# Kernel tuning notes

Hardware: AMD Instinct MI355X
Metric: run time of the kernel (lower is better)

## Reference

```python
import jax, jax.numpy as jnp
import numpy as np

N = 100000
E = 3200000
D = 128
H = 128
Q = 1000000
EPS = 1e-6


def _lin_params(key, fan_in, fan_out):
    k1, k2 = jax.random.split(key)
    bound = 1.0 / np.sqrt(fan_in)
    W = jax.random.uniform(k1, (fan_out, fan_in), jnp.float32, -bound, bound)
    b = jax.random.uniform(k2, (fan_out,), jnp.float32, -bound, bound)
    return W, b


def setup_inputs() -> dict:
    key = jax.random.key(0)
    ks = jax.random.split(key, 10)
    x = jax.random.normal(ks[0], (N, D), jnp.float32)
    edge_index = jax.random.randint(ks[1], (2, E), 0, N, jnp.int64)
    decode_index = jax.random.randint(ks[2], (2, Q), 0, N, jnp.int64)
    # SAGEConv1: lin_l (on aggregated neighbors, has bias) + lin_r (root, no bias)
    W1l, b1l = _lin_params(ks[3], D, H)
    W1r, _ = _lin_params(ks[4], D, H)
    W2l, b2l = _lin_params(ks[5], H, H)
    W2r, _ = _lin_params(ks[6], H, H)
    Wi, bi = _lin_params(ks[7], H, H)   # rnn.i2h
    Wh, bh = _lin_params(ks[8], H, H)   # rnn.h2h (applied to zero hidden -> bias only)
    Wo, bo = _lin_params(ks[9], H, H)   # rnn.h2o
    return {"x": x, "edge_index": edge_index, "decode_index": decode_index,
            "W1l": W1l, "b1l": b1l, "W1r": W1r,
            "W2l": W2l, "b2l": b2l, "W2r": W2r,
            "Wi": Wi, "bi": bi, "Wh": Wh, "bh": bh, "Wo": Wo, "bo": bo}


def _sage(x, src, dst, Wl, bl, Wr):
    # mean-aggregate source features onto targets, then lin_l(agg)+lin_r(x)
    msg = x[src]                                              # [E, d] gather
    agg = jax.ops.segment_sum(msg, dst, num_segments=N)       # [N, d] scatter-add
    cnt = jax.ops.segment_sum(jnp.ones((src.shape[0],), x.dtype), dst, num_segments=N)
    mean = agg / jnp.maximum(cnt, 1.0)[:, None]
    return mean @ Wl.T + bl + x @ Wr.T


def reference(x, edge_index, decode_index, W1l, b1l, W1r, W2l, b2l, W2r,
              Wi, bi, Wh, bh, Wo, bo):
    src, dst = edge_index[0], edge_index[1]
    h = jax.nn.relu(_sage(x, src, dst, W1l, b1l, W1r))
    # dropout is identity in eval mode
    h = _sage(h, src, dst, W2l, b2l, W2r)
    # RNN step: hidden is reset to zeros inside original forward, so h2h -> bias
    hid = jnp.tanh(h @ Wi.T + bi + bh)                        # [N, H]
    out = hid @ Wo.T + bo                                     # [N, H]
    a = out[decode_index[0]]                                  # [Q, H]
    b = out[decode_index[1]]
    na = jnp.maximum(jnp.linalg.norm(a, axis=1), EPS)
    nb = jnp.maximum(jnp.linalg.norm(b, axis=1), EPS)
    cos = jnp.sum(a * b, axis=1) / (na * nb)                  # [Q]
    return jax.nn.sigmoid(cos)
```

## Files before the change

### kernel.cpp

```cpp
#include <hip/hip_runtime.h>
#include <math.h>

#define DH 128
#define STILE 1024
#define BBLK 256
#define MAXK 512

typedef __attribute__((ext_vector_type(4))) float f32x4;
typedef __attribute__((ext_vector_type(8))) short short8;


__device__ __forceinline__ float lo2f(unsigned w) { return __uint_as_float(w << 16); }
__device__ __forceinline__ float hi2f(unsigned w) { return __uint_as_float(w & 0xFFFF0000u); }
__device__ __forceinline__ unsigned pack2bf(float a, float b) {
    unsigned ua = __float_as_uint(a), ub = __float_as_uint(b);
    unsigned ra = (ua + 0x7FFFu + ((ua >> 16) & 1u)) >> 16;
    unsigned rb = (ub + 0x7FFFu + ((ub >> 16) & 1u)) >> 16;
    return ra | (rb << 16);
}
__device__ __forceinline__ ushort bf16r(float f) {
    unsigned u = __float_as_uint(f);
    return (ushort)((u + 0x7FFFu + ((u >> 16) & 1u)) >> 16);
}

__global__ __launch_bounds__(256) void k_tobf(const float* __restrict__ in,
                                              uint4* __restrict__ outv, int n8) {
    int i = blockIdx.x * blockDim.x + threadIdx.x;
    if (i >= n8) return;
    const float4* p = reinterpret_cast<const float4*>(in);
    float4 a = p[i * 2], b = p[i * 2 + 1];
    uint4 w;
    w.x = pack2bf(a.x, a.y); w.y = pack2bf(a.z, a.w);
    w.z = pack2bf(b.x, b.y); w.w = pack2bf(b.z, b.w);
    outv[i] = w;
}


__global__ __launch_bounds__(512) void k_bhist(const int* __restrict__ ei,
                                               int* __restrict__ ghist,
                                               int E_, int K) {
    __shared__ int lh[MAXK];
    int tid = threadIdx.x, blk = blockIdx.x;
    if (tid < MAXK) lh[tid] = 0;
    __syncthreads();
    const int* dsts = ei + E_;
    int E4 = E_ >> 2;
    for (int e4 = blk * 512 + tid; e4 < E4; e4 += BBLK * 512) {
        int4 d4 = *reinterpret_cast<const int4*>(dsts + e4 * 4);
        atomicAdd(&lh[d4.x >> 8], 1);
        atomicAdd(&lh[d4.y >> 8], 1);
        atomicAdd(&lh[d4.z >> 8], 1);
        atomicAdd(&lh[d4.w >> 8], 1);
    }
    if (blk == 0 && tid < (E_ & 3)) atomicAdd(&lh[dsts[(E4 << 2) + tid] >> 8], 1);
    __syncthreads();
    if (tid < K) ghist[tid * BBLK + blk] = lh[tid];
}


__global__ __launch_bounds__(256) void k_scan1(const int* __restrict__ deg,
                                               int* __restrict__ excl,
                                               int* __restrict__ tsum, int N_) {
    __shared__ int wsum[4];
    int t = threadIdx.x;
    int idx = blockIdx.x * STILE + t * 4;
    int4 v = {0, 0, 0, 0};
    if (idx + 3 < N_) {
        v = *reinterpret_cast<const int4*>(deg + idx);
    } else {
        if (idx + 0 < N_) v.x = deg[idx + 0];
        if (idx + 1 < N_) v.y = deg[idx + 1];
        if (idx + 2 < N_) v.z = deg[idx + 2];
        if (idx + 3 < N_) v.w = deg[idx + 3];
    }
    int s0 = v.x, s1 = s0 + v.y, s2 = s1 + v.z, s3 = s2 + v.w;
    int lane = t & 63, w = t >> 6;
    int inc = s3;
    for (int off = 1; off < 64; off <<= 1) {
        int u = __shfl_up(inc, off, 64);
        if (lane >= off) inc += u;
    }
    if (lane == 63) wsum[w] = inc;
    __syncthreads();
    int woff = 0;
    for (int i = 0; i < w; ++i) woff += wsum[i];
    int exq = woff + inc - s3;
    int4 e;
    e.x = exq; e.y = exq + s0; e.z = exq + s1; e.w = exq + s2;
    if (idx + 3 < N_) {
        *reinterpret_cast<int4*>(excl + idx) = e;
    } else {
        if (idx + 0 < N_) excl[idx + 0] = e.x;
        if (idx + 1 < N_) excl[idx + 1] = e.y;
        if (idx + 2 < N_) excl[idx + 2] = e.z;
        if (idx + 3 < N_) excl[idx + 3] = e.w;
    }
    if (t == 255) tsum[blockIdx.x] = woff + inc;
}

__global__ void k_scan2(const int* __restrict__ tsum, int* __restrict__ toff,
                        int ntiles, int* __restrict__ totalOut) {
    __shared__ int sh[1024];
    int t = threadIdx.x;
    int v = (t < ntiles) ? tsum[t] : 0;
    sh[t] = v;
    __syncthreads();
    for (int off = 1; off < 1024; off <<= 1) {
        int u = (t >= off) ? sh[t - off] : 0;
        __syncthreads();
        sh[t] += u;
        __syncthreads();
    }
    if (t < ntiles) toff[t] = sh[t] - v;
    if (t == 1023) *totalOut = sh[1023];
}

__global__ __launch_bounds__(256) void k_scan3s(int* __restrict__ buf,
                                                const int* __restrict__ toff, int N_) {
    int off = toff[blockIdx.x];
    int idx = blockIdx.x * STILE + threadIdx.x * 4;
    if (idx + 3 < N_) {
        int4 e = *reinterpret_cast<int4*>(buf + idx);
        e.x += off; e.y += off; e.z += off; e.w += off;
        *reinterpret_cast<int4*>(buf + idx) = e;
    } else {
        for (int i = 0; i < 4; ++i)
            if (idx + i < N_) buf[idx + i] += off;
    }
}

__global__ __launch_bounds__(512) void k_bwrite(const int* __restrict__ ei,
                                                const int* __restrict__ goff,
                                                int2* __restrict__ ebuf,
                                                int E_, int K) {
    __shared__ int lcur[MAXK];
    int tid = threadIdx.x, blk = blockIdx.x;
    if (tid < K) lcur[tid] = goff[tid * BBLK + blk];
    __syncthreads();
    const int* dsts = ei + E_;
    int E4 = E_ >> 2;
    for (int e4 = blk * 512 + tid; e4 < E4; e4 += BBLK * 512) {
        int4 d4 = *reinterpret_cast<const int4*>(dsts + e4 * 4);
        int4 s4 = *reinterpret_cast<const int4*>(ei + e4 * 4);
        int p;
        p = atomicAdd(&lcur[d4.x >> 8], 1); ebuf[p] = make_int2(s4.x, d4.x);
        p = atomicAdd(&lcur[d4.y >> 8], 1); ebuf[p] = make_int2(s4.y, d4.y);
        p = atomicAdd(&lcur[d4.z >> 8], 1); ebuf[p] = make_int2(s4.z, d4.z);
        p = atomicAdd(&lcur[d4.w >> 8], 1); ebuf[p] = make_int2(s4.w, d4.w);
    }
    if (blk == 0 && tid < (E_ & 3)) {
        int e = (E4 << 2) + tid;
        int d = dsts[e];
        int p = atomicAdd(&lcur[d >> 8], 1);
        ebuf[p] = make_int2(ei[e], d);
    }
}

__global__ __launch_bounds__(256) void k_bscatter(const int2* __restrict__ ebuf,
                                                  const int* __restrict__ goff,
                                                  int* __restrict__ rowptr,
                                                  int* __restrict__ col,
                                                  int E_, int N_, int K) {
    __shared__ int ldeg[256], lrp[256], lcur[256], wsum[4];
    int b = blockIdx.x;
    int tid = threadIdx.x;
    int n0 = b << 8;
    int nn = min(256, N_ - n0);
    int estart = goff[b * BBLK];
    int eend = (b + 1 < K) ? goff[(b + 1) * BBLK] : E_;
    ldeg[tid] = 0;
    lcur[tid] = 0;
    __syncthreads();
    for (int e = estart + tid; e < eend; e += 256)
        atomicAdd(&ldeg[ebuf[e].y - n0], 1);
    __syncthreads();
    int v = ldeg[tid];
    int lane = tid & 63, w = tid >> 6;
    int inc = v;
    for (int off = 1; off < 64; off <<= 1) {
        int u = __shfl_up(inc, off, 64);
        if (lane >= off) inc += u;
    }
    if (lane == 63) wsum[w] = inc;
    __syncthreads();
    int woff = 0;
    for (int i = 0; i < w; ++i) woff += wsum[i];
    int rp = estart + woff + inc - v;
    lrp[tid] = rp;
    if (tid < nn) rowptr[n0 + tid] = rp;
    __syncthreads();
    for (int e = estart + tid; e < eend; e += 256) {
        int2 pr = ebuf[e];
        int dl = pr.y - n0;
        int p = lrp[dl] + atomicAdd(&lcur[dl], 1);
        col[p] = pr.x;
    }
}


__global__ __launch_bounds__(256) void k_prepw(const float* __restrict__ w0,
                                               const float* __restrict__ w1,
                                               const float* __restrict__ w2,
                                               const float* __restrict__ w3,
                                               const float* __restrict__ w4,
                                               const float* __restrict__ w5,
                                               ushort* __restrict__ wf) {
    int t = blockIdx.x * 256 + threadIdx.x;
    if (t >= 12288) return;
    int m = t >> 11;
    int rem = t & 2047;
    int kb = rem >> 9;
    int rem2 = rem & 511;
    int jb = rem2 >> 6;
    int l = rem2 & 63;
    const float* W;
    switch (m) {
        case 0: W = w0; break; case 1: W = w1; break; case 2: W = w2; break;
        case 3: W = w3; break; case 4: W = w4; break; default: W = w5; break;
    }
    int j = jb * 16 + (l & 15);
    int k0 = kb * 32 + (l >> 4) * 8;
    const float* src = W + (size_t)j * DH + k0;
    uint4 o;
    o.x = pack2bf(src[0], src[1]);
    o.y = pack2bf(src[2], src[3]);
    o.z = pack2bf(src[4], src[5]);
    o.w = pack2bf(src[6], src[7]);
    *reinterpret_cast<uint4*>(wf + (size_t)t * 8) = o;
}


__global__ __launch_bounds__(256) void k_agg_bf(const uint2* __restrict__ Fv,
                                                const int* __restrict__ rowptr,
                                                const int* __restrict__ col,
                                                uint2* __restrict__ out, int N_) {
    int g = (blockIdx.x * blockDim.x + threadIdx.x) >> 5;
    int l = threadIdx.x & 31;
    if (g >= N_) return;
    int lo = rowptr[g], hi = rowptr[g + 1];
    float4 acc0 = {0.f, 0.f, 0.f, 0.f};
    float4 acc1 = {0.f, 0.f, 0.f, 0.f};
    float4 acc2 = {0.f, 0.f, 0.f, 0.f};
    float4 acc3 = {0.f, 0.f, 0.f, 0.f};
    int j = lo;
    for (; j + 3 < hi; j += 4) {
        int s0 = col[j], s1 = col[j + 1], s2 = col[j + 2], s3 = col[j + 3];
        uint2 v0 = Fv[(size_t)s0 * 32 + l];
        uint2 v1 = Fv[(size_t)s1 * 32 + l];
        uint2 v2 = Fv[(size_t)s2 * 32 + l];
        uint2 v3 = Fv[(size_t)s3 * 32 + l];
        acc0.x += lo2f(v0.x); acc0.y += hi2f(v0.x); acc0.z += lo2f(v0.y); acc0.w += hi2f(v0.y);
        acc1.x += lo2f(v1.x); acc1.y += hi2f(v1.x); acc1.z += lo2f(v1.y); acc1.w += hi2f(v1.y);
        acc2.x += lo2f(v2.x); acc2.y += hi2f(v2.x); acc2.z += lo2f(v2.y); acc2.w += hi2f(v2.y);
        acc3.x += lo2f(v3.x); acc3.y += hi2f(v3.x); acc3.z += lo2f(v3.y); acc3.w += hi2f(v3.y);
    }
    for (; j < hi; ++j) {
        uint2 v0 = Fv[(size_t)col[j] * 32 + l];
        acc0.x += lo2f(v0.x); acc0.y += hi2f(v0.x); acc0.z += lo2f(v0.y); acc0.w += hi2f(v0.y);
    }
    float inv = 1.0f / fmaxf((float)(hi - lo), 1.0f);
    float rx = (acc0.x + acc1.x + acc2.x + acc3.x) * inv;
    float ry = (acc0.y + acc1.y + acc2.y + acc3.y) * inv;
    float rz = (acc0.z + acc1.z + acc2.z + acc3.z) * inv;
    float rw = (acc0.w + acc1.w + acc2.w + acc3.w) * inv;
    uint2 w;
    w.x = pack2bf(rx, ry);
    w.y = pack2bf(rz, rw);
    out[(size_t)g * 32 + l] = w;
}


template <int ACT>
__global__ __launch_bounds__(256) void k_mfma_dual(const ushort* __restrict__ A,
                                                   const ushort* __restrict__ B,
                                                   const ushort* __restrict__ WaF,
                                                   const ushort* __restrict__ WbF,
                                                   const float* __restrict__ bias,
                                                   ushort* __restrict__ out, int N_) {
    int wv = threadIdx.x >> 6;
    int l  = threadIdx.x & 63;
    int base = blockIdx.x * 64 + wv * 16;
    if (base >= N_) return;
    int l15 = l & 15, g = l >> 4;
    f32x4 acc[8];
#pragma unroll
    for (int jb = 0; jb < 8; ++jb) {
        float b = bias[jb * 16 + l15];
        acc[jb] = (f32x4){b, b, b, b};
    }
    const ushort* arow = A + (size_t)(base + l15) * DH + g * 8;
    const ushort* brow = B + (size_t)(base + l15) * DH + g * 8;
#pragma unroll
    for (int kb = 0; kb < 4; ++kb) {
        short8 aA = *reinterpret_cast<const short8*>(arow + kb * 32);
        short8 aB = *reinterpret_cast<const short8*>(brow + kb * 32);
        const ushort* wa = WaF + kb * 4096 + l * 8;
        const ushort* wb = WbF + kb * 4096 + l * 8;
#pragma unroll
        for (int jb = 0; jb < 8; ++jb) {
            short8 fa = *reinterpret_cast<const short8*>(wa + jb * 512);
            short8 fb = *reinterpret_cast<const short8*>(wb + jb * 512);
            acc[jb] = __builtin_amdgcn_mfma_f32_16x16x32_bf16(aA, fa, acc[jb], 0, 0, 0);
            acc[jb] = __builtin_amdgcn_mfma_f32_16x16x32_bf16(aB, fb, acc[jb], 0, 0, 0);
        }
    }
    ushort* orow = out + (size_t)(base + g * 4) * DH + l15;
#pragma unroll
    for (int jb = 0; jb < 8; ++jb) {
#pragma unroll
        for (int r = 0; r < 4; ++r) {
            float v = acc[jb][r];
            if (ACT) v = fmaxf(v, 0.f);
            orow[(size_t)r * DH + jb * 16] = bf16r(v);
        }
    }
}


__global__ __launch_bounds__(256) void k_rnn_mfma(const ushort* __restrict__ H2,
                                                  const ushort* __restrict__ WiF,
                                                  const float* __restrict__ bi,
                                                  const float* __restrict__ bh,
                                                  const ushort* __restrict__ WoF,
                                                  const float* __restrict__ bo,
                                                  ushort* __restrict__ out, int N_) {
    __shared__ ushort lds[4][16][136];
    int wv = threadIdx.x >> 6;
    int l  = threadIdx.x & 63;
    int base = blockIdx.x * 64 + wv * 16;
    if (base >= N_) return;
    int l15 = l & 15, g = l >> 4;
    f32x4 acc[8];
#pragma unroll
    for (int jb = 0; jb < 8; ++jb) {
        float b = bi[jb * 16 + l15] + bh[jb * 16 + l15];
        acc[jb] = (f32x4){b, b, b, b};
    }
    const ushort* arow = H2 + (size_t)(base + l15) * DH + g * 8;
#pragma unroll
    for (int kb = 0; kb < 4; ++kb) {
        short8 a = *reinterpret_cast<const short8*>(arow + kb * 32);
        const ushort* wi = WiF + kb * 4096 + l * 8;
#pragma unroll
        for (int jb = 0; jb < 8; ++jb) {
            short8 f = *reinterpret_cast<const short8*>(wi + jb * 512);
            acc[jb] = __builtin_amdgcn_mfma_f32_16x16x32_bf16(a, f, acc[jb], 0, 0, 0);
        }
    }
#pragma unroll
    for (int jb = 0; jb < 8; ++jb)
#pragma unroll
        for (int r = 0; r < 4; ++r)
            lds[wv][g * 4 + r][jb * 16 + l15] = bf16r(tanhf(acc[jb][r]));
#pragma unroll
    for (int jb = 0; jb < 8; ++jb) {
        float b = bo[jb * 16 + l15];
        acc[jb] = (f32x4){b, b, b, b};
    }
#pragma unroll
    for (int kb = 0; kb < 4; ++kb) {
        short8 a = *reinterpret_cast<const short8*>(&lds[wv][l15][kb * 32 + g * 8]);
        const ushort* wo = WoF + kb * 4096 + l * 8;
#pragma unroll
        for (int jb = 0; jb < 8; ++jb) {
            short8 f = *reinterpret_cast<const short8*>(wo + jb * 512);
            acc[jb] = __builtin_amdgcn_mfma_f32_16x16x32_bf16(a, f, acc[jb], 0, 0, 0);
        }
    }
#pragma unroll
    for (int r = 0; r < 4; ++r) {
        float ss = 0.f;
#pragma unroll
        for (int jb = 0; jb < 8; ++jb) ss += acc[jb][r] * acc[jb][r];
        ss += __shfl_xor(ss, 1);
        ss += __shfl_xor(ss, 2);
        ss += __shfl_xor(ss, 4);
        ss += __shfl_xor(ss, 8);
        float inv = 1.0f / fmaxf(sqrtf(ss), 1e-6f);
        ushort* orow = out + (size_t)(base + g * 4 + r) * DH + l15;
#pragma unroll
        for (int jb = 0; jb < 8; ++jb)
            orow[jb * 16] = bf16r(acc[jb][r] * inv);
    }
}


__global__ __launch_bounds__(256) void k_decode(const uint2* __restrict__ Fn,
                                                const int* __restrict__ di,
                                                float* __restrict__ res, int Q_) {
    int q = (blockIdx.x * blockDim.x + threadIdx.x) >> 5;
    int l = threadIdx.x & 31;
    if (q >= Q_) return;
    int ia = di[q];
    int ib = di[Q_ + q];
    uint2 a = Fn[(size_t)ia * 32 + l];
    uint2 b = Fn[(size_t)ib * 32 + l];
    float s = lo2f(a.x) * lo2f(b.x) + hi2f(a.x) * hi2f(b.x)
            + lo2f(a.y) * lo2f(b.y) + hi2f(a.y) * hi2f(b.y);
#pragma unroll
    for (int off = 16; off; off >>= 1) s += __shfl_xor(s, off, 32);
    if (l == 0) res[q] = 1.0f / (1.0f + expf(-s));
}


extern "C" void kernel_launch(void* const* d_in, const int* in_sizes, int n_in,
                              void* d_out, int out_size, void* d_ws, size_t ws_size,
                              hipStream_t stream) {
    const float* x   = (const float*)d_in[0];
    const int*   ei  = (const int*)d_in[1];
    const int*   di  = (const int*)d_in[2];
    const float* W1l = (const float*)d_in[3];
    const float* b1l = (const float*)d_in[4];
    const float* W1r = (const float*)d_in[5];
    const float* W2l = (const float*)d_in[6];
    const float* b2l = (const float*)d_in[7];
    const float* W2r = (const float*)d_in[8];
    const float* Wi  = (const float*)d_in[9];
    const float* bi  = (const float*)d_in[10];
    const float* bh  = (const float*)d_in[12];
    const float* Wo  = (const float*)d_in[13];
    const float* bo  = (const float*)d_in[14];
    float* outq = (float*)d_out;

    int N_ = in_sizes[0] / DH;
    int E_ = in_sizes[1] / 2;
    int Q_ = in_sizes[2] / 2;
    int K  = (N_ + 255) >> 8;
    int GH = K * BBLK;
    int gtiles = (GH + STILE - 1) / STILE;

    char* base = (char*)d_ws;
    size_t o = 0;
    auto alloc = [&](size_t bytes) -> void* {
        o = (o + 511) & ~(size_t)511;
        void* p = base + o;
        o += bytes;
        return p;
    };
    int*    rowptr = (int*)alloc((size_t)(N_ + 1) * 4);
    int*    col    = (int*)alloc((size_t)E_ * 4);
    int*    ghist  = (int*)alloc((size_t)GH * 4);
    int*    goff   = (int*)alloc((size_t)GH * 4);
    int2*   ebuf   = (int2*)alloc((size_t)E_ * 8);
    int*    tsum   = (int*)alloc((size_t)1024 * 4);
    int*    toff   = (int*)alloc((size_t)1024 * 4);
    ushort* wf     = (ushort*)alloc((size_t)6 * 16384 * 2);
    void*   xbf    = alloc((size_t)N_ * DH * 2);
    void*   hbf    = alloc((size_t)N_ * DH * 2);
    void*   aggbf  = alloc((size_t)N_ * DH * 2);
    void*   h2bf   = alloc((size_t)N_ * DH * 2);
    void*   outbf  = alloc((size_t)N_ * DH * 2);

    k_tobf<<<(N_ * DH / 8 + 255) / 256, 256, 0, stream>>>(x, (uint4*)xbf, N_ * DH / 8);
    k_bhist<<<BBLK, 512, 0, stream>>>(ei, ghist, E_, K);
    k_scan1<<<gtiles, 256, 0, stream>>>(ghist, goff, tsum, GH);
    k_scan2<<<1, 1024, 0, stream>>>(tsum, toff, gtiles, rowptr + N_);
    k_scan3s<<<gtiles, 256, 0, stream>>>(goff, toff, GH);
    k_bwrite<<<BBLK, 512, 0, stream>>>(ei, goff, ebuf, E_, K);
    k_bscatter<<<K, 256, 0, stream>>>(ebuf, goff, rowptr, col, E_, N_, K);
    k_prepw<<<48, 256, 0, stream>>>(W1l, W1r, W2l, W2r, Wi, Wo, wf);

    int gw = (N_ + 63) / 64;
    k_agg_bf<<<(N_ + 7) / 8, 256, 0, stream>>>((const uint2*)xbf, rowptr, col, (uint2*)aggbf, N_);
    k_mfma_dual<1><<<gw, 256, 0, stream>>>((const ushort*)aggbf, (const ushort*)xbf,
                                           wf + 0 * 16384, wf + 1 * 16384, b1l,
                                           (ushort*)hbf, N_);
    k_agg_bf<<<(N_ + 7) / 8, 256, 0, stream>>>((const uint2*)hbf, rowptr, col, (uint2*)aggbf, N_);
    k_mfma_dual<0><<<gw, 256, 0, stream>>>((const ushort*)aggbf, (const ushort*)hbf,
                                           wf + 2 * 16384, wf + 3 * 16384, b2l,
                                           (ushort*)h2bf, N_);
    k_rnn_mfma<<<gw, 256, 0, stream>>>((const ushort*)h2bf, wf + 4 * 16384, bi, bh,
                                       wf + 5 * 16384, bo, (ushort*)outbf, N_);
    k_decode<<<(Q_ + 7) / 8, 256, 0, stream>>>((const uint2*)outbf, di, outq, Q_);
}
```

Measured before the change: 609.5 us.

## Store gathered node features in FP8 for aggregation and decode gathers

Converts the node feature tables read by the neighbor-aggregation gathers and the decode gathers from bf16 to 8-bit e4m3 floats. The x conversion kernel now also emits an fp8 copy, a new pass quantizes the layer-1 output to fp8, and the RNN kernel writes its normalized output in fp8. This halves the bytes moved by the random-access gathers, which dominate memory traffic. The cost is an extra quantization pass and much lower precision in the aggregated means and cosine scores, which may exceed tolerance.

New measurement: 519.0 us. 1.17x faster.

```diff
diff --git a/kernel.cpp b/kernel.cpp
--- a/kernel.cpp
+++ b/kernel.cpp
@@ -7,7 +7,14 @@
 #define MAXK 512
 
 typedef __attribute__((ext_vector_type(4))) float f32x4;
+typedef __attribute__((ext_vector_type(2))) float f32x2;
 typedef __attribute__((ext_vector_type(8))) short short8;
+
+#if __has_builtin(__builtin_amdgcn_cvt_pk_f32_fp8) && __has_builtin(__builtin_amdgcn_cvt_pk_fp8_f32)
+#define HAVE_HW_FP8 1
+#else
+#define HAVE_HW_FP8 0
+#endif
 
 
 __device__ __forceinline__ float lo2f(unsigned w) { return __uint_as_float(w << 16); }
@@ -23,8 +30,60 @@
     return (ushort)((u + 0x7FFFu + ((u >> 16) & 1u)) >> 16);
 }
 
+
+__device__ __forceinline__ float fp8tof(unsigned v) {
+    return __uint_as_float(((v & 0x80u) << 24) | ((v & 0x7Fu) << 20)) * 0x1p120f;
+}
+
+__device__ __forceinline__ unsigned f2fp8(float f) {
+    unsigned s = (__float_as_uint(f) >> 24) & 0x80u;
+    float a = fabsf(f);
+    if (a > 448.0f) a = 448.0f;
+    if (a < 0x1p-10f) return s;
+    int e = (int)((__float_as_uint(a) >> 23) & 0xFF) - 127;
+    if (e < -6) {
+        unsigned m = (unsigned)rintf(a * 512.0f);
+        return s | m;
+    }
+    unsigned ua = __float_as_uint(a);
+    unsigned em = (unsigned)(((e + 7) << 3) | ((ua >> 20) & 7u));
+    unsigned rest = ua & 0xFFFFFu;
+    em += (rest > 0x80000u) || (rest == 0x80000u && (em & 1u));
+    if (em > 0x7Eu) em = 0x7Eu;
+    return s | em;
+}
+
+__device__ __forceinline__ unsigned pack4q(float x0, float x1, float x2, float x3) {
+#if HAVE_HW_FP8
+    int v = __builtin_amdgcn_cvt_pk_fp8_f32(x0, x1, 0, false);
+    v = __builtin_amdgcn_cvt_pk_fp8_f32(x2, x3, v, true);
+    return (unsigned)v;
+#else
+    return f2fp8(x0) | (f2fp8(x1) << 8) | (f2fp8(x2) << 16) | (f2fp8(x3) << 24);
+#endif
+}
+
+__device__ __forceinline__ void unpack4q(unsigned u, float& f0, float& f1, float& f2, float& f3) {
+#if HAVE_HW_FP8
+    f32x2 lo = __builtin_amdgcn_cvt_pk_f32_fp8((int)u, false);
+    f32x2 hi = __builtin_amdgcn_cvt_pk_f32_fp8((int)u, true);
+    f0 = lo[0]; f1 = lo[1]; f2 = hi[0]; f3 = hi[1];
+#else
+    f0 = fp8tof(u); f1 = fp8tof(u >> 8); f2 = fp8tof(u >> 16); f3 = fp8tof(u >> 24);
+#endif
+}
+
+__device__ __forceinline__ unsigned f2q1(float v) {
+#if HAVE_HW_FP8
+    return (unsigned)__builtin_amdgcn_cvt_pk_fp8_f32(v, v, 0, false) & 0xFFu;
+#else
+    return f2fp8(v);
+#endif
+}
+
 __global__ __launch_bounds__(256) void k_tobf(const float* __restrict__ in,
-                                              uint4* __restrict__ outv, int n8) {
+                                              uint4* __restrict__ outbf,
+                                              uint2* __restrict__ outq, int n8) {
     int i = blockIdx.x * blockDim.x + threadIdx.x;
     if (i >= n8) return;
     const float4* p = reinterpret_cast<const float4*>(in);
@@ -32,7 +91,19 @@
     uint4 w;
     w.x = pack2bf(a.x, a.y); w.y = pack2bf(a.z, a.w);
     w.z = pack2bf(b.x, b.y); w.w = pack2bf(b.z, b.w);
-    outv[i] = w;
+    outbf[i] = w;
+    uint2 q;
+    q.x = pack4q(a.x, a.y, a.z, a.w);
+    q.y = pack4q(b.x, b.y, b.z, b.w);
+    outq[i] = q;
+}
+
+__global__ __launch_bounds__(256) void k_bf2q(const uint2* __restrict__ inb,
+                                              unsigned* __restrict__ outq, int n4) {
+    int i = blockIdx.x * blockDim.x + threadIdx.x;
+    if (i >= n4) return;
+    uint2 v = inb[i];
+    outq[i] = pack4q(lo2f(v.x), hi2f(v.x), lo2f(v.y), hi2f(v.y));
 }
 
 
@@ -56,7 +127,6 @@
     __syncthreads();
     if (tid < K) ghist[tid * BBLK + blk] = lh[tid];
 }
-
 
 __global__ __launch_bounds__(256) void k_scan1(const int* __restrict__ deg,
                                                int* __restrict__ excl,
@@ -230,10 +300,10 @@
 }
 
 
-__global__ __launch_bounds__(256) void k_agg_bf(const uint2* __restrict__ Fv,
-                                                const int* __restrict__ rowptr,
-                                                const int* __restrict__ col,
-                                                uint2* __restrict__ out, int N_) {
+__global__ __launch_bounds__(256) void k_agg_q(const unsigned* __restrict__ Fq,
+                                               const int* __restrict__ rowptr,
+                                               const int* __restrict__ col,
+                                               uint2* __restrict__ out, int N_) {
     int g = (blockIdx.x * blockDim.x + threadIdx.x) >> 5;
     int l = threadIdx.x & 31;
     if (g >= N_) return;
@@ -245,18 +315,25 @@
     int j = lo;
     for (; j + 3 < hi; j += 4) {
         int s0 = col[j], s1 = col[j + 1], s2 = col[j + 2], s3 = col[j + 3];
-        uint2 v0 = Fv[(size_t)s0 * 32 + l];
-        uint2 v1 = Fv[(size_t)s1 * 32 + l];
-        uint2 v2 = Fv[(size_t)s2 * 32 + l];
-        uint2 v3 = Fv[(size_t)s3 * 32 + l];
-        acc0.x += lo2f(v0.x); acc0.y += hi2f(v0.x); acc0.z += lo2f(v0.y); acc0.w += hi2f(v0.y);
-        acc1.x += lo2f(v1.x); acc1.y += hi2f(v1.x); acc1.z += lo2f(v1.y); acc1.w += hi2f(v1.y);
-        acc2.x += lo2f(v2.x); acc2.y += hi2f(v2.x); acc2.z += lo2f(v2.y); acc2.w += hi2f(v2.y);
-        acc3.x += lo2f(v3.x); acc3.y += hi2f(v3.x); acc3.z += lo2f(v3.y); acc3.w += hi2f(v3.y);
+        unsigned v0 = Fq[(size_t)s0 * 32 + l];
+        unsigned v1 = Fq[(size_t)s1 * 32 + l];
+        unsigned v2 = Fq[(size_t)s2 * 32 + l];
+        unsigned v3 = Fq[(size_t)s3 * 32 + l];
+        float f0, f1, f2, f3;
+        unpack4q(v0, f0, f1, f2, f3);
+        acc0.x += f0; acc0.y += f1; acc0.z += f2; acc0.w += f3;
+        unpack4q(v1, f0, f1, f2, f3);
+        acc1.x += f0; acc1.y += f1; acc1.z += f2; acc1.w += f3;
+        unpack4q(v2, f0, f1, f2, f3);
+        acc2.x += f0; acc2.y += f1; acc2.z += f2; acc2.w += f3;
+        unpack4q(v3, f0, f1, f2, f3);
+        acc3.x += f0; acc3.y += f1; acc3.z += f2; acc3.w += f3;
     }
     for (; j < hi; ++j) {
-        uint2 v0 = Fv[(size_t)col[j] * 32 + l];
-        acc0.x += lo2f(v0.x); acc0.y += hi2f(v0.x); acc0.z += lo2f(v0.y); acc0.w += hi2f(v0.y);
+        unsigned v0 = Fq[(size_t)col[j] * 32 + l];
+        float f0, f1, f2, f3;
+        unpack4q(v0, f0, f1, f2, f3);
+        acc0.x += f0; acc0.y += f1; acc0.z += f2; acc0.w += f3;
     }
     float inv = 1.0f / fmaxf((float)(hi - lo), 1.0f);
     float rx = (acc0.x + acc1.x + acc2.x + acc3.x) * inv;
@@ -323,7 +400,7 @@
                                                   const float* __restrict__ bh,
                                                   const ushort* __restrict__ WoF,
                                                   const float* __restrict__ bo,
-                                                  ushort* __restrict__ out, int N_) {
+                                                  unsigned char* __restrict__ outq, int N_) {
     __shared__ ushort lds[4][16][136];
     int wv = threadIdx.x >> 6;
     int l  = threadIdx.x & 63;
@@ -377,15 +454,15 @@
         ss += __shfl_xor(ss, 4);
         ss += __shfl_xor(ss, 8);
         float inv = 1.0f / fmaxf(sqrtf(ss), 1e-6f);
-        ushort* orow = out + (size_t)(base + g * 4 + r) * DH + l15;
+        unsigned char* orow = outq + (size_t)(base + g * 4 + r) * DH + l15;
 #pragma unroll
         for (int jb = 0; jb < 8; ++jb)
-            orow[jb * 16] = bf16r(acc[jb][r] * inv);
-    }
-}
-
-
-__global__ __launch_bounds__(256) void k_decode(const uint2* __restrict__ Fn,
+            orow[jb * 16] = (unsigned char)f2q1(acc[jb][r] * inv);
+    }
+}
+
+
+__global__ __launch_bounds__(256) void k_decode(const unsigned* __restrict__ Fq,
                                                 const int* __restrict__ di,
                                                 float* __restrict__ res, int Q_) {
     int q = (blockIdx.x * blockDim.x + threadIdx.x) >> 5;
@@ -393,10 +470,12 @@
     if (q >= Q_) return;
     int ia = di[q];
     int ib = di[Q_ + q];
-    uint2 a = Fn[(size_t)ia * 32 + l];
-    uint2 b = Fn[(size_t)ib * 32 + l];
-    float s = lo2f(a.x) * lo2f(b.x) + hi2f(a.x) * hi2f(b.x)
-            + lo2f(a.y) * lo2f(b.y) + hi2f(a.y) * hi2f(b.y);
+    unsigned a = Fq[(size_t)ia * 32 + l];
+    unsigned b = Fq[(size_t)ib * 32 + l];
+    float a0, a1, a2, a3, b0, b1, b2, b3;
+    unpack4q(a, a0, a1, a2, a3);
+    unpack4q(b, b0, b1, b2, b3);
+    float s = a0 * b0 + a1 * b1 + a2 * b2 + a3 * b3;
 #pragma unroll
     for (int off = 16; off; off >>= 1) s += __shfl_xor(s, off, 32);
     if (l == 0) res[q] = 1.0f / (1.0f + expf(-s));
@@ -449,9 +528,12 @@
     void*   hbf    = alloc((size_t)N_ * DH * 2);
     void*   aggbf  = alloc((size_t)N_ * DH * 2);
     void*   h2bf   = alloc((size_t)N_ * DH * 2);
-    void*   outbf  = alloc((size_t)N_ * DH * 2);
-
-    k_tobf<<<(N_ * DH / 8 + 255) / 256, 256, 0, stream>>>(x, (uint4*)xbf, N_ * DH / 8);
+    void*   xq     = alloc((size_t)N_ * DH);
+    void*   hq     = alloc((size_t)N_ * DH);
+    void*   oq     = alloc((size_t)N_ * DH);
+
+    k_tobf<<<(N_ * DH / 8 + 255) / 256, 256, 0, stream>>>(x, (uint4*)xbf, (uint2*)xq,
+                                                          N_ * DH / 8);
     k_bhist<<<BBLK, 512, 0, stream>>>(ei, ghist, E_, K);
     k_scan1<<<gtiles, 256, 0, stream>>>(ghist, goff, tsum, GH);
     k_scan2<<<1, 1024, 0, stream>>>(tsum, toff, gtiles, rowptr + N_);
@@ -461,15 +543,19 @@
     k_prepw<<<48, 256, 0, stream>>>(W1l, W1r, W2l, W2r, Wi, Wo, wf);
 
     int gw = (N_ + 63) / 64;
-    k_agg_bf<<<(N_ + 7) / 8, 256, 0, stream>>>((const uint2*)xbf, rowptr, col, (uint2*)aggbf, N_);
+    k_agg_q<<<(N_ + 7) / 8, 256, 0, stream>>>((const unsigned*)xq, rowptr, col,
+                                              (uint2*)aggbf, N_);
     k_mfma_dual<1><<<gw, 256, 0, stream>>>((const ushort*)aggbf, (const ushort*)xbf,
                                            wf + 0 * 16384, wf + 1 * 16384, b1l,
                                            (ushort*)hbf, N_);
-    k_agg_bf<<<(N_ + 7) / 8, 256, 0, stream>>>((const uint2*)hbf, rowptr, col, (uint2*)aggbf, N_);
+    k_bf2q<<<(N_ * DH / 4 + 255) / 256, 256, 0, stream>>>((const uint2*)hbf,
+                                                          (unsigned*)hq, N_ * DH / 4);
+    k_agg_q<<<(N_ + 7) / 8, 256, 0, stream>>>((const unsigned*)hq, rowptr, col,
+                                              (uint2*)aggbf, N_);
     k_mfma_dual<0><<<gw, 256, 0, stream>>>((const ushort*)aggbf, (const ushort*)hbf,
                                            wf + 2 * 16384, wf + 3 * 16384, b2l,
                                            (ushort*)h2bf, N_);
     k_rnn_mfma<<<gw, 256, 0, stream>>>((const ushort*)h2bf, wf + 4 * 16384, bi, bh,
-                                       wf + 5 * 16384, bo, (ushort*)outbf, N_);
-    k_decode<<<(Q_ + 7) / 8, 256, 0, stream>>>((const uint2*)outbf, di, outq, Q_);
-}
+                                       wf + 5 * 16384, bo, (unsigned char*)oq, N_);
+    k_decode<<<(Q_ + 7) / 8, 256, 0, stream>>>((const unsigned*)oq, di, outq, Q_);
+}
```
